# Kernel tuning notes

Hardware: AMD Instinct MI355X
Metric: run time of the kernel (lower is better)

Reference implementation:

```python
import jax, jax.numpy as jnp
import numpy as np

NUM_CLASSES = 1000
TEMPERATURE = 0.1
B, B_OOD, D = 4096, 4096, 512


def _l2norm(x):
    return x / jnp.linalg.norm(x, axis=-1, keepdims=True)


def setup_inputs() -> dict:
    key = jax.random.key(0)
    k1, k2, k3, k4, k5 = jax.random.split(key, 5)
    return {
        "centers1": _l2norm(jax.random.normal(k1, (NUM_CLASSES, D), dtype=jnp.float32)),
        "features": _l2norm(jax.random.normal(k2, (B, D), dtype=jnp.float32)),
        "targets": jax.random.randint(k3, (B,), 0, NUM_CLASSES, dtype=jnp.int64 if jax.config.jax_enable_x64 else jnp.int32),
        "features_ood": _l2norm(jax.random.normal(k4, (B_OOD, D), dtype=jnp.float32)),
        "pseudo_target_ood": jax.random.randint(k5, (B_OOD,), 0, NUM_CLASSES, dtype=jnp.int64 if jax.config.jax_enable_x64 else jnp.int32),
    }


def reference(centers1, features, targets, features_ood, pseudo_target_ood):
    C = centers1.shape[0]
    b = features.shape[0]
    bo = features_ood.shape[0]
    n = b + C + bo  # total anchors: batch + class centers + ood

    centers_lbl = jnp.arange(C, dtype=targets.dtype)
    ood_lbl = jnp.full((bo,), C, dtype=targets.dtype)  # ood gets label == num_classes
    targets_all = jnp.concatenate([targets, centers_lbl, ood_lbl])              # [N]
    targets_all_class = jnp.concatenate([targets, centers_lbl, pseudo_target_ood])  # [N]

    # per-class count over all N labels (pseudo labels for ood)
    batch_cls_count = jnp.zeros((C,), dtype=jnp.float32).at[targets_all_class].add(1.0)

    # positive mask: same label as anchor, excluding self (diagonal for j < B)
    mask = (targets_all[:b, None] == targets_all[None, :]).astype(jnp.float32)  # [B,N]
    logits_mask = 1.0 - (jnp.arange(n)[None, :] == jnp.arange(b)[:, None]).astype(jnp.float32)
    mask = mask * logits_mask

    features_all = jnp.concatenate([features, centers1, features_ood], axis=0)  # [N,D]
    logits = jnp.matmul(features, features_all.T) / TEMPERATURE                 # [B,N]
    logits = logits - jax.lax.stop_gradient(jnp.max(logits, axis=1, keepdims=True))

    exp_logits = jnp.exp(logits) * logits_mask
    # class-balanced per-instance weight (count of the column's class, minus positive mask)
    per_ins_weight = batch_cls_count[targets_all_class][None, :] - mask         # [B,N]
    exp_logits_sum = jnp.sum(exp_logits / per_ins_weight, axis=1, keepdims=True)
    log_prob = logits - jnp.log(exp_logits_sum)

    mean_log_prob_pos = jnp.sum(mask * log_prob, axis=1) / jnp.sum(mask, axis=1)
    loss = -jnp.mean(mean_log_prob_pos)
    return loss
```

## Files before the change

### kernel.cpp

```cpp
#include <hip/hip_runtime.h>
#include <stdint.h>

#define NUM_C 1000
#define NB    4096
#define NCOL  9192
#define NPAD  9216
#define DK    512
#define BM    128
#define BN    256
#define INV_T 10.0f

typedef __attribute__((ext_vector_type(16))) float f32x16;
typedef __attribute__((ext_vector_type(8)))  int   i32x8;

union frag8 { i32x8 v; uint4 q[2]; };

#define OFF_FALL  0u
#define OFF_CNT   4718592u
#define OFF_CNTT  4722688u
#define OFF_S     4726784u
#define OFF_P     4743168u

#define NCHUNKBLK 1152

__device__ __forceinline__ void async16(const void* g, void* l) {
  __builtin_amdgcn_global_load_lds((const __attribute__((address_space(1))) void*)g,
                                   (__attribute__((address_space(3))) void*)l,
                                   16, 0, 0);
}

__device__ __forceinline__ unsigned sw_e4m3(float x) {
  float ax = fabsf(x);
  unsigned s = (__float_as_uint(x) >> 24) & 0x80u;
  if (ax < 0.015625f) {
    int n = (int)rintf(ax * 512.0f);
    if (n >= 8) return s | 0x08u;
    return s | (unsigned)n;
  }
  if (ax >= 448.0f) return s | 0x7Eu;
  unsigned u = __float_as_uint(ax);
  int ee = (int)(u >> 23) - 127;
  float scale = __uint_as_float((unsigned)(3 - ee + 127) << 23);
  int qv = (int)rintf(ax * scale);
  if (qv == 16) { ee++; qv = 8; }
  return s | (unsigned)(((ee + 7) << 3) | (qv - 8));
}

template <bool HI>
__device__ __forceinline__ int cvt2(float a, float b, int old) {
#if __has_builtin(__builtin_amdgcn_cvt_pk_fp8_f32)
  return __builtin_amdgcn_cvt_pk_fp8_f32(a, b, old, HI);
#else
  unsigned pk = sw_e4m3(a) | (sw_e4m3(b) << 8);
  return HI ? (int)(((unsigned)old & 0x0000FFFFu) | (pk << 16))
            : (int)(((unsigned)old & 0xFFFF0000u) | pk);
#endif
}

#define MFMA_SC(a, b, c) \
  __builtin_amdgcn_mfma_scale_f32_32x32x64_f8f6f4((a), (b), (c), 0, 0, 0, 0x7F7F7F7F, 0, 0x7F7F7F7F)

__global__ __launch_bounds__(256) void prep_k(const float* __restrict__ centers,
                                              const float* __restrict__ feats,
                                              const float* __restrict__ ood,
                                              const int* __restrict__ targets,
                                              const int* __restrict__ pseudo,
                                              uint4* __restrict__ fall,
                                              unsigned* __restrict__ cnt,
                                              unsigned* __restrict__ cntT,
                                              float* __restrict__ SP) {
  __shared__ unsigned hc[1024];
  __shared__ unsigned hct[1024];
  const int tid = threadIdx.x;

  if (blockIdx.x > 0) {
    int idx  = (blockIdx.x - 1) * 256 + tid;
    int tile = idx >> 10;
    int kq   = (idx >> 7) & 7;
    int p    = idx & 127;
    int c    = p ^ ((p >> 3) & 7);
    int lane = c >> 1;
    int row  = tile * 32 + (lane & 31);
    int k0   = kq * 64 + (lane >> 5) * 32 + (c & 1) * 16;

    const float* src = nullptr;
    if (row < NB)              src = feats   + (size_t)row * DK;
    else if (row < NB + NUM_C) src = centers + (size_t)(row - NB) * DK;
    else if (row < NCOL)       src = ood     + (size_t)(row - NB - NUM_C) * DK;
    uint4 out = make_uint4(0u, 0u, 0u, 0u);
    if (src) {
      float4 v0 = *(const float4*)(src + k0);
      float4 v1 = *(const float4*)(src + k0 + 4);
      float4 v2 = *(const float4*)(src + k0 + 8);
      float4 v3 = *(const float4*)(src + k0 + 12);
      int q;
      q = 0; q = cvt2<false>(v0.x, v0.y, q); q = cvt2<true>(v0.z, v0.w, q); out.x = (unsigned)q;
      q = 0; q = cvt2<false>(v1.x, v1.y, q); q = cvt2<true>(v1.z, v1.w, q); out.y = (unsigned)q;
      q = 0; q = cvt2<false>(v2.x, v2.y, q); q = cvt2<true>(v2.z, v2.w, q); out.z = (unsigned)q;
      q = 0; q = cvt2<false>(v3.x, v3.y, q); q = cvt2<true>(v3.z, v3.w, q); out.w = (unsigned)q;
    }
    fall[idx] = out;

    if (blockIdx.x <= 32)
      SP[(blockIdx.x - 1) * 256 + tid] = 0.0f;
  } else {
    for (int kk = tid; kk < 1024; kk += 256) { hc[kk] = 0u; hct[kk] = 0u; }
    __syncthreads();
    for (int i = tid; i < NB; i += 256) {
      int tt = targets[i];
      atomicAdd(&hc[tt], 1u);
      atomicAdd(&hct[tt], 1u);
      atomicAdd(&hc[pseudo[i]], 1u);
    }
    __syncthreads();
    for (int kk = tid; kk < 1024; kk += 256) {
      cnt[kk]  = hc[kk];
      cntT[kk] = hct[kk];
    }
  }
}

__global__ __launch_bounds__(512, 4) void gemm_fused(const unsigned char* __restrict__ fall,
                                                     const int* __restrict__ targets,
                                                     const int* __restrict__ pseudo,
                                                     const unsigned* __restrict__ cnt,
                                                     float* __restrict__ Sacc,
                                                     float* __restrict__ Pacc) {
  __shared__ unsigned char Alds[65536];
  __shared__ int4   sTab[BN];
  __shared__ int    sTgt[BM];
  __shared__ float  sS[BM];
  __shared__ float  sP[BM];

  const int tid  = threadIdx.x;
  int flat = (int)blockIdx.y * 36 + (int)blockIdx.x;
  int swz  = (flat & 7) * 144 + (flat >> 3);
  const int nTile = swz >> 5;
  const int mTile = swz & 31;
  const int lane  = tid & 63;
  const int wv    = tid >> 6;
  const int wm    = wv >> 2;
  const int wn    = wv & 3;

  {
    const unsigned char* aSrc = fall + (size_t)mTile * 65536;
#pragma unroll
    for (int i = 0; i < 8; i++)
      async16(aSrc + (i * 512 + tid) * 16, &Alds[(i * 512 + tid) * 16]);
  }

  if (tid < BN) {
    int j = nTile * BN + tid;
    int lbl, tac;
    if (j >= NCOL)         { lbl = -1; tac = -1; }
    else if (j < NB)       { tac = targets[j]; lbl = tac; }
    else if (j < NB+NUM_C) { tac = j - NB;     lbl = tac; }
    else                   { tac = pseudo[j - NB - NUM_C]; lbl = NUM_C; }
    float r0 = 0.f, r1 = 0.f;
    if (tac >= 0) {
      float w = (float)(1u + cnt[tac]);
      r0 = 1.0f / w;
      r1 = 1.0f / (w - 1.0f);
    }
    sTab[tid] = make_int4(lbl, __float_as_int(r0), __float_as_int(r1), 0);
  } else if (tid < BN + BM) {
    int i = tid - BN;
    sTgt[i] = targets[mTile * BM + i];
    sS[i] = 0.f;
    sP[i] = 0.f;
  }

  const int swzo = ((lane >> 2) & 7) << 4;
  const int off0 = (lane << 5) ^ swzo;
  const int off1 = off0 ^ 16;

  const unsigned char* bBase0 = fall + (size_t)(nTile * 8 + wn * 2) * 16384;
  const unsigned char* bBase1 = bBase0 + 16384;

  frag8 b0p, b1p, b0q, b1q;
  b0p.q[0] = *(const uint4*)(bBase0 + off0);
  b0p.q[1] = *(const uint4*)(bBase0 + off1);
  b1p.q[0] = *(const uint4*)(bBase1 + off0);
  b1p.q[1] = *(const uint4*)(bBase1 + off1);
  b0q.q[0] = *(const uint4*)(bBase0 + 2048 + off0);
  b0q.q[1] = *(const uint4*)(bBase0 + 2048 + off1);
  b1q.q[0] = *(const uint4*)(bBase1 + 2048 + off0);
  b1q.q[1] = *(const uint4*)(bBase1 + 2048 + off1);

  f32x16 acc00, acc01, acc10, acc11;
  {
    f32x16 z;
#pragma unroll
    for (int t = 0; t < 16; t++) z[t] = 0.f;
    acc00 = z; acc01 = z; acc10 = z; acc11 = z;
  }

  const unsigned aRow0 = (unsigned)(wm * 2 + 0) * 16384u;
  const unsigned aRow1 = (unsigned)(wm * 2 + 1) * 16384u;

  __syncthreads();

#pragma unroll
  for (int k2 = 0; k2 < 4; k2++) {
    const unsigned ke = (unsigned)(2 * k2) * 2048u;
    const unsigned ko = ke + 2048u;
    {
      frag8 a0, a1;
      a0.q[0] = *(const uint4*)&Alds[aRow0 + ke + off0];
      a0.q[1] = *(const uint4*)&Alds[aRow0 + ke + off1];
      a1.q[0] = *(const uint4*)&Alds[aRow1 + ke + off0];
      a1.q[1] = *(const uint4*)&Alds[aRow1 + ke + off1];
      acc00 = MFMA_SC(b0p.v, a0.v, acc00);
      acc01 = MFMA_SC(b1p.v, a0.v, acc01);
      acc10 = MFMA_SC(b0p.v, a1.v, acc10);
      acc11 = MFMA_SC(b1p.v, a1.v, acc11);
      if (k2 < 3) {
        b0p.q[0] = *(const uint4*)(bBase0 + (ke + 4096u) + off0);
        b0p.q[1] = *(const uint4*)(bBase0 + (ke + 4096u) + off1);
        b1p.q[0] = *(const uint4*)(bBase1 + (ke + 4096u) + off0);
        b1p.q[1] = *(const uint4*)(bBase1 + (ke + 4096u) + off1);
      }
    }
    {
      frag8 a0, a1;
      a0.q[0] = *(const uint4*)&Alds[aRow0 + ko + off0];
      a0.q[1] = *(const uint4*)&Alds[aRow0 + ko + off1];
      a1.q[0] = *(const uint4*)&Alds[aRow1 + ko + off0];
      a1.q[1] = *(const uint4*)&Alds[aRow1 + ko + off1];
      acc00 = MFMA_SC(b0q.v, a0.v, acc00);
      acc01 = MFMA_SC(b1q.v, a0.v, acc01);
      acc10 = MFMA_SC(b0q.v, a1.v, acc10);
      acc11 = MFMA_SC(b1q.v, a1.v, acc11);
      if (k2 < 3) {
        b0q.q[0] = *(const uint4*)(bBase0 + (ko + 4096u) + off0);
        b0q.q[1] = *(const uint4*)(bBase0 + (ko + 4096u) + off1);
        b1q.q[0] = *(const uint4*)(bBase1 + (ko + 4096u) + off0);
        b1q.q[1] = *(const uint4*)(bBase1 + (ko + 4096u) + off1);
      }
    }
  }

  const int cq = lane & 31;
  const int hh = lane >> 5;
  const int iloc0 = wm * 64 + cq;
  const int iloc1 = iloc0 + 32;
  const int ig0 = mTile * BM + iloc0;
  const int ig1 = mTile * BM + iloc1;
  const int ti0 = sTgt[iloc0];
  const int ti1 = sTgt[iloc1];

  float s0 = 0.f, s1 = 0.f, p0 = 0.f, p1 = 0.f;
#pragma unroll
  for (int nj = 0; nj < 2; nj++) {
#pragma unroll
    for (int r = 0; r < 16; r++) {
      int jl = wn * 64 + nj * 32 + (r & 3) + 8 * (r >> 2) + 4 * hh;
      int jg = nTile * BN + jl;
      int4 tb = sTab[jl];
      float rw0 = __int_as_float(tb.y);
      float rw1 = __int_as_float(tb.z);
      float a0 = nj ? acc01[r] : acc00[r];
      float a1 = nj ? acc11[r] : acc10[r];
      {
        bool d = (jg == ig0);
        bool pp = (tb.x == ti0) && !d;
        float rw = d ? 0.f : (pp ? rw1 : rw0);
        float e = __expf(fmaf(a0, INV_T, -INV_T));
        s0 = fmaf(e, rw, s0);
        p0 += pp ? a0 : 0.f;
      }
      {
        bool d = (jg == ig1);
        bool pp = (tb.x == ti1) && !d;
        float rw = d ? 0.f : (pp ? rw1 : rw0);
        float e = __expf(fmaf(a1, INV_T, -INV_T));
        s1 = fmaf(e, rw, s1);
        p1 += pp ? a1 : 0.f;
      }
    }
  }
  atomicAdd(&sS[iloc0], s0);
  atomicAdd(&sP[iloc0], p0 * INV_T);
  atomicAdd(&sS[iloc1], s1);
  atomicAdd(&sP[iloc1], p1 * INV_T);

  __syncthreads();
  if (tid < BM) {
    int ig = mTile * BM + tid;
    atomicAdd(&Sacc[ig], sS[tid]);
    atomicAdd(&Pacc[ig], sP[tid]);
  }
}

__global__ __launch_bounds__(256) void finalize_k(const float* __restrict__ S,
                                                  const float* __restrict__ P,
                                                  const int* __restrict__ targets,
                                                  const unsigned* __restrict__ cntT,
                                                  float* __restrict__ out) {
  __shared__ unsigned ct[1024];
  __shared__ float red[4];
  int tid = threadIdx.x;
  for (int k = tid; k < 1024; k += 256) ct[k] = cntT[k];
  __syncthreads();
  float local = 0.f;
  for (int i = tid; i < NB; i += 256) {
    float npos = (float)ct[targets[i]];
    local += P[i] / npos - INV_T - __logf(S[i]);
  }
  for (int m = 1; m < 64; m <<= 1) local += __shfl_xor(local, m, 64);
  if ((tid & 63) == 0) red[tid >> 6] = local;
  __syncthreads();
  if (tid == 0) {
    float t = red[0] + red[1] + red[2] + red[3];
    out[0] = -t / (float)NB;
  }
}

extern "C" void kernel_launch(void* const* d_in, const int* in_sizes, int n_in,
                              void* d_out, int out_size, void* d_ws, size_t ws_size,
                              hipStream_t stream) {
  const float* centers = (const float*)d_in[0];
  const float* feats   = (const float*)d_in[1];
  const int*   targets = (const int*)d_in[2];
  const float* ood     = (const float*)d_in[3];
  const int*   pseudo  = (const int*)d_in[4];

  char* ws = (char*)d_ws;
  uint4*    fall  = (uint4*)(ws + OFF_FALL);
  unsigned* cnt   = (unsigned*)(ws + OFF_CNT);
  unsigned* cntT  = (unsigned*)(ws + OFF_CNTT);
  float*    Sacc  = (float*)(ws + OFF_S);
  float*    Pacc  = (float*)(ws + OFF_P);

  prep_k<<<dim3(NCHUNKBLK + 1), 256, 0, stream>>>(centers, feats, ood, targets, pseudo,
                                                  fall, cnt, cntT, Sacc);
  gemm_fused<<<dim3(NPAD / BN, NB / BM), 512, 0, stream>>>((const unsigned char*)fall, targets,
                                                           pseudo, cnt, Sacc, Pacc);
  finalize_k<<<1, 256, 0, stream>>>(Sacc, Pacc, targets, cntT, (float*)d_out);
}
```

Before: 123.5 us.

## Double GEMM column tile to 512 with 1024-thread blocks and per-wave LDS reduction

Widens each block's column tile from 256 to 512 and moves to 1024-thread blocks with 16 waves, so every A tile loaded into LDS is reused across twice as many columns and the grid is half as large. The shared-memory atomics for the row sums are replaced by a cross-half-wave shuffle, per-wave LDS slots, and a final serial sum over eight waves. The risks are lower occupancy from 1024-thread blocks under launch_bounds(1024,4) and register pressure. The wave-to-tile mapping (wm, wn) and tile swizzle are also reworked, which depends on code not shown, such as hh and iloc.

```diff
diff --git a/kernel.cpp b/kernel.cpp
--- a/kernel.cpp
+++ b/kernel.cpp
@@ -7,7 +7,7 @@
 #define NPAD  9216
 #define DK    512
 #define BM    128
-#define BN    256
+#define BN    512
 #define INV_T 10.0f
 
 typedef __attribute__((ext_vector_type(16))) float f32x16;
@@ -120,33 +120,33 @@
   }
 }
 
-__global__ __launch_bounds__(512, 4) void gemm_fused(const unsigned char* __restrict__ fall,
-                                                     const int* __restrict__ targets,
-                                                     const int* __restrict__ pseudo,
-                                                     const unsigned* __restrict__ cnt,
-                                                     float* __restrict__ Sacc,
-                                                     float* __restrict__ Pacc) {
+__global__ __launch_bounds__(1024, 4) void gemm_fused(const unsigned char* __restrict__ fall,
+                                                      const int* __restrict__ targets,
+                                                      const int* __restrict__ pseudo,
+                                                      const unsigned* __restrict__ cnt,
+                                                      float* __restrict__ Sacc,
+                                                      float* __restrict__ Pacc) {
   __shared__ unsigned char Alds[65536];
   __shared__ int4   sTab[BN];
   __shared__ int    sTgt[BM];
-  __shared__ float  sS[BM];
-  __shared__ float  sP[BM];
+  __shared__ float  sSw[8][BM];
+  __shared__ float  sPw[8][BM];
 
   const int tid  = threadIdx.x;
-  int flat = (int)blockIdx.y * 36 + (int)blockIdx.x;
-  int swz  = (flat & 7) * 144 + (flat >> 3);
+  int flat = (int)blockIdx.x;
+  int swz  = (flat & 7) * 72 + (flat >> 3);
   const int nTile = swz >> 5;
   const int mTile = swz & 31;
   const int lane  = tid & 63;
   const int wv    = tid >> 6;
-  const int wm    = wv >> 2;
-  const int wn    = wv & 3;
+  const int wm    = wv & 1;
+  const int wn    = wv >> 1;
 
   {
     const unsigned char* aSrc = fall + (size_t)mTile * 65536;
 #pragma unroll
-    for (int i = 0; i < 8; i++)
-      async16(aSrc + (i * 512 + tid) * 16, &Alds[(i * 512 + tid) * 16]);
+    for (int i = 0; i < 4; i++)
+      async16(aSrc + (i * 1024 + tid) * 16, &Alds[(i * 1024 + tid) * 16]);
   }
 
   if (tid < BN) {
@@ -164,17 +164,14 @@
     }
     sTab[tid] = make_int4(lbl, __float_as_int(r0), __float_as_int(r1), 0);
   } else if (tid < BN + BM) {
-    int i = tid - BN;
-    sTgt[i] = targets[mTile * BM + i];
-    sS[i] = 0.f;
-    sP[i] = 0.f;
+    sTgt[tid - BN] = targets[mTile * BM + (tid - BN)];
   }
 
   const int swzo = ((lane >> 2) & 7) << 4;
   const int off0 = (lane << 5) ^ swzo;
   const int off1 = off0 ^ 16;
 
-  const unsigned char* bBase0 = fall + (size_t)(nTile * 8 + wn * 2) * 16384;
+  const unsigned char* bBase0 = fall + (size_t)(nTile * 16 + wn * 2) * 16384;
   const unsigned char* bBase1 = bBase0 + 16384;
 
   frag8 b0p, b1p, b0q, b1q;
@@ -279,16 +276,25 @@
       }
     }
   }
-  atomicAdd(&sS[iloc0], s0);
-  atomicAdd(&sP[iloc0], p0 * INV_T);
-  atomicAdd(&sS[iloc1], s1);
-  atomicAdd(&sP[iloc1], p1 * INV_T);
+  s0 += __shfl_xor(s0, 32, 64);
+  s1 += __shfl_xor(s1, 32, 64);
+  p0 += __shfl_xor(p0, 32, 64);
+  p1 += __shfl_xor(p1, 32, 64);
+  if (hh == 0) {
+    sSw[wn][iloc0] = s0;
+    sSw[wn][iloc1] = s1;
+    sPw[wn][iloc0] = p0 * INV_T;
+    sPw[wn][iloc1] = p1 * INV_T;
+  }
 
   __syncthreads();
   if (tid < BM) {
+    float S = 0.f, P = 0.f;
+#pragma unroll
+    for (int w = 0; w < 8; w++) { S += sSw[w][tid]; P += sPw[w][tid]; }
     int ig = mTile * BM + tid;
-    atomicAdd(&Sacc[ig], sS[tid]);
-    atomicAdd(&Pacc[ig], sP[tid]);
+    atomicAdd(&Sacc[ig], S);
+    atomicAdd(&Pacc[ig], P);
   }
 }
 
@@ -334,7 +340,8 @@
 
   prep_k<<<dim3(NCHUNKBLK + 1), 256, 0, stream>>>(centers, feats, ood, targets, pseudo,
                                                   fall, cnt, cntT, Sacc);
-  gemm_fused<<<dim3(NPAD / BN, NB / BM), 512, 0, stream>>>((const unsigned char*)fall, targets,
-                                                           pseudo, cnt, Sacc, Pacc);
+  gemm_fused<<<dim3((NPAD / BN) * (NB / BM)), 1024, 0, stream>>>((const unsigned char*)fall,
+                                                                 targets, pseudo, cnt,
+                                                                 Sacc, Pacc);
   finalize_k<<<1, 256, 0, stream>>>(Sacc, Pacc, targets, cntT, (float*)d_out);
 }
```

Measured after the change: 120.3 us. -2.6%, faster.
